# Kernel optimization log

Measured on AMD Instinct MI355X. Metric: run time of the kernel, lower is better.

## Reference

```python
import jax, jax.numpy as jnp
import numpy as np

N_HEADS = 16


def setup_inputs() -> dict:
    key = jax.random.key(0)
    ks = jax.random.split(key, 8)
    ts, td, b, hc = 64, 4096, 8, 1024
    scale = 1.0 / np.sqrt(hc)
    return {
        "s": jax.random.normal(ks[0], (ts, b, hc), dtype=jnp.float32),
        "d": jax.random.normal(ks[1], (td, b, hc), dtype=jnp.float32),
        "Wq": jax.random.normal(ks[2], (hc, hc), dtype=jnp.float32) * scale,
        "bq": jax.random.normal(ks[3], (hc,), dtype=jnp.float32) * 0.01,
        "Wk": jax.random.normal(ks[4], (hc, hc), dtype=jnp.float32) * scale,
        "bk": jax.random.normal(ks[5], (hc,), dtype=jnp.float32) * 0.01,
        "Wv": jax.random.normal(ks[6], (hc, hc), dtype=jnp.float32) * scale,
        "bv": jax.random.normal(ks[7], (hc,), dtype=jnp.float32) * 0.01,
    }


def reference(s, d, Wq, bq, Wk, bk, Wv, bv):
    ts, b, hc = s.shape
    td = d.shape[0]
    h = N_HEADS
    c = hc // h
    # linear projections (torch Linear: x @ W.T + b)
    q = (s @ Wq.T + bq).reshape(ts, b, h, c)
    k = (d @ Wk.T + bk).reshape(td, b, h, c)
    v = (d @ Wv.T + bv).reshape(td, b, h, c)
    # scores over (slot, token) pairs, scaled
    a = jnp.einsum('sbhc,dbhc->sdbh', q, k) / jnp.sqrt(jnp.asarray(c, s.dtype))
    # competitive softmax across the SLOT axis (dim 0), not the key axis
    a = jax.nn.softmax(a, axis=0)          # (ts, td, b, h)
    n = jnp.sum(a, axis=1) + 0.001         # (ts, b, h)
    num = jnp.einsum('sdbh,dbhc->sbhc', a, v)
    out = num / n[..., None]               # normalized weighted average
    return out.reshape(ts, b, hc)
```

## Files before the change

kernel.cpp:

```cpp
#include <hip/hip_runtime.h>


#define TS 64
#define TD 4096
#define BATCH 8
#define HC 1024
#define NHEAD 16
#define MD (TD*BATCH)
#define MS (TS*BATCH)
#define NCHUNK 8
#define CHTOK (TD/NCHUNK)

typedef __attribute__((ext_vector_type(8))) __bf16 bf16x8;
typedef __attribute__((ext_vector_type(4))) float f32x4;
typedef __attribute__((ext_vector_type(4))) unsigned short u16x4;
typedef __attribute__((ext_vector_type(8))) unsigned short u16x8;

__device__ __forceinline__ unsigned short f2bf(float x){
  union { float f; unsigned u; } v; v.f = x;
  unsigned r = v.u + 0x7FFFu + ((v.u >> 16) & 1u);
  return (unsigned short)(r >> 16);
}

__device__ __forceinline__ void gll16(const void* g, void* l){
  __builtin_amdgcn_global_load_lds((__attribute__((address_space(1))) void*)g,
                                   (__attribute__((address_space(3))) void*)l, 16, 0, 0);
}

__global__ void cvt_all(const float* __restrict__ d, const float* __restrict__ s,
                        const float* __restrict__ wq, const float* __restrict__ wk,
                        const float* __restrict__ wv,
                        unsigned short* __restrict__ dbf, unsigned short* __restrict__ sbf,
                        unsigned short* __restrict__ wqb, unsigned short* __restrict__ wkb,
                        unsigned short* __restrict__ wvb){
  long i = (long)blockIdx.x * 256 + threadIdx.x;
  const float* src; unsigned short* dst; long off;
  if (i < 8388608L)      { src = d;  dst = dbf; off = i; }
  else if (i < 8519680L) { src = s;  dst = sbf; off = i - 8388608L; }
  else if (i < 8781824L) { src = wq; dst = wqb; off = i - 8519680L; }
  else if (i < 9043968L) { src = wk; dst = wkb; off = i - 8781824L; }
  else                   { src = wv; dst = wvb; off = i - 9043968L; }
  f32x4 f = ((const f32x4*)src)[off];
  u16x4 o;
  o[0] = f2bf(f[0]); o[1] = f2bf(f[1]); o[2] = f2bf(f[2]); o[3] = f2bf(f[3]);
  ((u16x4*)dst)[off] = o;
}

__global__ __launch_bounds__(256, 2) void gemm_kv(
    const unsigned short* __restrict__ A,
    const unsigned short* __restrict__ W,
    const float* __restrict__ bk,
    const float* __restrict__ bv,
    unsigned short* __restrict__ Kout,
    unsigned short* __restrict__ Vout)
{
  __shared__ unsigned short As[2][256*32];
  __shared__ unsigned short Bs[2][128*32];

  const int nwg = gridDim.x;
  const int cpx = nwg >> 3;
  const int orig = blockIdx.x;
  const int wg = (orig & 7) * cpx + (orig >> 3);
  const int mt = wg >> 4, nt = wg & 15;
  const int tid = threadIdx.x;
  const int lane = tid & 63, w = tid >> 6;
  const int l15 = lane & 15, lg = lane >> 4;
  const int wm = w >> 1, wn = w & 1;

  const int srow = lane >> 2;
  const unsigned schunk = (unsigned)(((lane & 3) ^ ((lane >> 3) & 3)) << 4);
  const char* aS = (const char*)A + (size_t)(mt*256) * 2048 + schunk;
  const char* bS = (const char*)W + (size_t)(nt*128) * 2048 + schunk;
  const unsigned ar0 = (unsigned)((  0 + w*16 + srow) * 2048);
  const unsigned ar1 = (unsigned)(( 64 + w*16 + srow) * 2048);
  const unsigned ar2 = (unsigned)((128 + w*16 + srow) * 2048);
  const unsigned ar3 = (unsigned)((192 + w*16 + srow) * 2048);
  const unsigned br0 = ar0, br1 = ar1;
  const unsigned da0 = (unsigned)((  0 + w*16) * 64);
  const unsigned da1 = (unsigned)(( 64 + w*16) * 64);
  const unsigned da2 = (unsigned)((128 + w*16) * 64);
  const unsigned da3 = (unsigned)((192 + w*16) * 64);

  #define STAGE(t_, buf_) { \
    const size_t ko = (size_t)(t_) * 64; \
    char* dA = (char*)&As[buf_][0]; char* dB = (char*)&Bs[buf_][0]; \
    gll16(aS + ar0 + ko, dA + da0); \
    gll16(aS + ar1 + ko, dA + da1); \
    gll16(aS + ar2 + ko, dA + da2); \
    gll16(aS + ar3 + ko, dA + da3); \
    gll16(bS + br0 + ko, dB + da0); \
    gll16(bS + br1 + ko, dB + da1); \
    __builtin_amdgcn_sched_barrier(0); }

  const unsigned ksel = (unsigned)((lg ^ ((l15 >> 1) & 3)) << 4);
  const unsigned aoff = (unsigned)(wm*128 + l15) * 64 + ksel;
  const unsigned boff = (unsigned)(wn*64  + l15) * 64 + ksel;

  const f32x4 fz = {0.f, 0.f, 0.f, 0.f};
  f32x4 acc[8][4];
  #pragma unroll
  for (int m = 0; m < 8; ++m)
    #pragma unroll
    for (int n = 0; n < 4; ++n) acc[m][n] = fz;

  #define TILE(buf_) { \
    const char* as_ = (const char*)&As[buf_][0]; \
    const char* bs_ = (const char*)&Bs[buf_][0]; \
    bf16x8 af[8], bf[4]; \
    _Pragma("unroll") \
    for (int m = 0; m < 8; ++m) af[m] = *(const bf16x8*)(as_ + aoff + m*1024u); \
    _Pragma("unroll") \
    for (int n = 0; n < 4; ++n) bf[n] = *(const bf16x8*)(bs_ + boff + n*1024u); \
    __builtin_amdgcn_s_setprio(1); \
    _Pragma("unroll") \
    for (int m = 0; m < 8; ++m) \
      _Pragma("unroll") \
      for (int n = 0; n < 4; ++n) \
        acc[m][n] = __builtin_amdgcn_mfma_f32_16x16x32_bf16(af[m], bf[n], acc[m][n], 0, 0, 0); \
    __builtin_amdgcn_s_setprio(0); }

  STAGE(0, 0)
  __syncthreads();

  #pragma unroll 1
  for (int tp = 0; tp < 16; ++tp){
    STAGE(2*tp + 1, 1)
    TILE(0)
    __syncthreads();
    if (tp < 15) STAGE(2*tp + 2, 0)
    TILE(1)
    __syncthreads();
  }

  const int ccol = (nt & 7)*128 + wn*64;
  unsigned short* Cb = (nt < 8) ? Kout : Vout;
  const float* bias = (nt < 8) ? bk : bv;
  float bvv[4];
  #pragma unroll
  for (int nf = 0; nf < 4; ++nf) bvv[nf] = bias[ccol + nf*16 + l15];
  #pragma unroll
  for (int mf = 0; mf < 8; ++mf){
    #pragma unroll
    for (int r = 0; r < 4; ++r){
      size_t row = (size_t)(mt*256 + wm*128 + mf*16 + lg*4 + r);
      unsigned short* cp = Cb + row*1024 + ccol;
      #pragma unroll
      for (int nf = 0; nf < 4; ++nf)
        cp[nf*16 + l15] = f2bf(acc[mf][nf][r] + bvv[nf]);
    }
  }
  #undef STAGE
  #undef TILE
}

__global__ __launch_bounds__(256) void gemm128(
    const unsigned short* __restrict__ A,
    const unsigned short* __restrict__ W,
    const float* __restrict__ bias,
    unsigned short* __restrict__ C)
{
  __shared__ unsigned short As[128*64];
  __shared__ unsigned short Bs[128*64];
  const int nwg = gridDim.x;
  const int cpx = nwg >> 3;
  const int orig = blockIdx.x;
  const int wg = (orig & 7) * cpx + (orig >> 3);
  const int mt = wg >> 3, nt = wg & 7;
  const int tid = threadIdx.x;
  const int lane = tid & 63, w = tid >> 6;
  const int l15 = lane & 15, lg = lane >> 4;
  const int wr = w >> 1, wc = w & 1;

  const int lrow = lane >> 3;
  const int lch  = (lane & 7) << 4;
  const char* pA[4]; const char* pB[4]; unsigned ldsoff[4];
  #pragma unroll
  for (int j = 0; j < 4; ++j){
    int row = w*32 + j*8 + lrow;
    int sw  = lch ^ ((row & 7) << 4);
    pA[j] = (const char*)A + (size_t)(mt*128 + row) * 2048 + sw;
    pB[j] = (const char*)W + (size_t)(nt*128 + row) * 2048 + sw;
    ldsoff[j] = (unsigned)(w*32 + j*8) * 128;
  }

  const f32x4 fz = {0.f, 0.f, 0.f, 0.f};
  f32x4 acc[4][4];
  #pragma unroll
  for (int m = 0; m < 4; ++m)
    #pragma unroll
    for (int n = 0; n < 4; ++n) acc[m][n] = fz;

  for (int kt = 0; kt < 16; ++kt){
    __syncthreads();
    #pragma unroll
    for (int j = 0; j < 4; ++j){
      gll16(pA[j] + (size_t)kt*128, (char*)As + ldsoff[j]);
      gll16(pB[j] + (size_t)kt*128, (char*)Bs + ldsoff[j]);
    }
    __syncthreads();
    #pragma unroll
    for (int kk = 0; kk < 2; ++kk){
      bf16x8 af[4], bfr[4];
      #pragma unroll
      for (int m = 0; m < 4; ++m){
        int row = wr*64 + m*16 + l15;
        af[m] = *(const bf16x8*)((const char*)As + row*128 + ((lg*16 + kk*64) ^ ((row & 7) << 4)));
      }
      #pragma unroll
      for (int n = 0; n < 4; ++n){
        int row = wc*64 + n*16 + l15;
        bfr[n] = *(const bf16x8*)((const char*)Bs + row*128 + ((lg*16 + kk*64) ^ ((row & 7) << 4)));
      }
      #pragma unroll
      for (int m = 0; m < 4; ++m)
        #pragma unroll
        for (int n = 0; n < 4; ++n)
          acc[m][n] = __builtin_amdgcn_mfma_f32_16x16x32_bf16(af[m], bfr[n], acc[m][n], 0, 0, 0);
    }
  }

  const int ccol0 = nt*128 + wc*64;
  float bv[4];
  #pragma unroll
  for (int n = 0; n < 4; ++n) bv[n] = bias[ccol0 + n*16 + l15];
  #pragma unroll
  for (int m = 0; m < 4; ++m){
    #pragma unroll
    for (int r = 0; r < 4; ++r){
      size_t row = (size_t)(mt*128 + wr*64 + m*16 + lg*4 + r);
      unsigned short* cp = C + row*1024 + ccol0;
      #pragma unroll
      for (int n = 0; n < 4; ++n)
        cp[n*16 + l15] = f2bf(acc[m][n][r] + bv[n]);
    }
  }
}

__global__ __launch_bounds__(256) void attn_kernel(
    const unsigned short* __restrict__ Q,
    const unsigned short* __restrict__ K,
    const unsigned short* __restrict__ V,
    float* __restrict__ P)
{
  __shared__ unsigned short Qs[64*64];
  __shared__ unsigned short Ks[64*64];
  __shared__ unsigned short Vt[80*64];
  __shared__ unsigned short Al[64*64];
  __shared__ float red[256];

  const int bh = blockIdx.x;
  const int chunk = blockIdx.y;
  const int bb = bh >> 4, h = bh & 15;
  const int tid = threadIdx.x;
  const int lane = tid & 63, w = tid >> 6;
  const int l15 = lane & 15, lg = lane >> 4;
  const int lrow = lane >> 3, lch = (lane & 7) << 4;

  for (int i = tid; i < 16*64; i += 256){
    int r = i >> 6;
    Vt[(64 + r)*64 + (i & 63)] = (r == 0) ? (unsigned short)0x3F80 : (unsigned short)0;
  }

  #pragma unroll
  for (int j = 0; j < 2; ++j){
    int row = w*16 + j*8 + lrow;
    int sw = lch ^ ((row & 7) << 4);
    const char* g = (const char*)Q + (size_t)(row*BATCH + bb)*2048 + h*128 + sw;
    gll16(g, (char*)Qs + (w*16 + j*8)*128);
  }

  const f32x4 fz = {0.f, 0.f, 0.f, 0.f};
  f32x4 acc[5];
  #pragma unroll
  for (int nb = 0; nb < 5; ++nb) acc[nb] = fz;

  const int vtok = tid >> 2;
  const int vcg  = tid & 3;
  const int t0 = chunk * CHTOK;

  for (int tt = 0; tt < CHTOK/64; ++tt){
    const int tb = t0 + tt*64;
    #pragma unroll
    for (int j = 0; j < 2; ++j){
      int row = w*16 + j*8 + lrow;
      int sw = lch ^ ((row & 7) << 4);
      const char* g = (const char*)K + (size_t)((size_t)(tb + row)*BATCH + bb)*2048 + h*128 + sw;
      gll16(g, (char*)Ks + (w*16 + j*8)*128);
    }
    const char* vg = (const char*)V + (size_t)((size_t)(tb + vtok)*BATCH + bb)*2048 + h*128 + vcg*32;
    u16x8 v0 = *(const u16x8*)vg;
    u16x8 v1 = *(const u16x8*)(vg + 16);
    __syncthreads();

    bf16x8 qa[2];
    #pragma unroll
    for (int kk = 0; kk < 2; ++kk){
      int row = w*16 + l15;
      qa[kk] = *(const bf16x8*)((const char*)Qs + row*128 + ((lg*16 + kk*64) ^ ((row & 7) << 4)));
    }
    float e[4][4];
    #pragma unroll
    for (int nb = 0; nb < 4; ++nb){
      f32x4 s = fz;
      #pragma unroll
      for (int kk = 0; kk < 2; ++kk){
        int row = nb*16 + l15;
        bf16x8 kb = *(const bf16x8*)((const char*)Ks + row*128 + ((lg*16 + kk*64) ^ ((row & 7) << 4)));
        s = __builtin_amdgcn_mfma_f32_16x16x32_bf16(qa[kk], kb, s, 0, 0, 0);
      }
      #pragma unroll
      for (int r = 0; r < 4; ++r) e[nb][r] = __expf(s[r] * 0.125f);
    }
    #pragma unroll
    for (int nb = 0; nb < 4; ++nb){
      float cp = e[nb][0] + e[nb][1] + e[nb][2] + e[nb][3];
      cp += __shfl_xor(cp, 16);
      cp += __shfl_xor(cp, 32);
      if (lg == 0) red[w*64 + nb*16 + l15] = cp;
    }
    __syncthreads();

    #pragma unroll
    for (int nb = 0; nb < 4; ++nb){
      int col = nb*16 + l15;
      float dn = red[col] + red[64 + col] + red[128 + col] + red[192 + col];
      float inv = 1.0f / dn;
      #pragma unroll
      for (int r = 0; r < 4; ++r){
        int row = w*16 + lg*4 + r;
        Al[row*64 + ((((2*col)) ^ ((row & 7) << 4)) >> 1)] = f2bf(e[nb][r] * inv);
      }
    }
    #pragma unroll
    for (int ee = 0; ee < 8; ++ee){
      int c0 = vcg*16 + ee;
      int sw0 = (((c0 & 7) ^ (c0 >> 3)) & 7) << 4;
      Vt[c0*64 + (((2*vtok) ^ sw0) >> 1)] = v0[ee];
    }
    #pragma unroll
    for (int ee = 0; ee < 8; ++ee){
      int c1 = vcg*16 + 8 + ee;
      int sw1 = (((c1 & 7) ^ (c1 >> 3)) & 7) << 4;
      Vt[c1*64 + (((2*vtok) ^ sw1) >> 1)] = v1[ee];
    }
    __syncthreads();

    bf16x8 aa[2];
    #pragma unroll
    for (int kk = 0; kk < 2; ++kk){
      int row = w*16 + l15;
      aa[kk] = *(const bf16x8*)((const char*)Al + row*128 + ((lg*16 + kk*64) ^ ((row & 7) << 4)));
    }
    #pragma unroll
    for (int nb = 0; nb < 5; ++nb){
      #pragma unroll
      for (int kk = 0; kk < 2; ++kk){
        int row = nb*16 + l15;
        int sw = (((row & 7) ^ (row >> 3)) & 7) << 4;
        bf16x8 vb = *(const bf16x8*)((const char*)Vt + row*128 + ((lg*16 + kk*64) ^ sw));
        acc[nb] = __builtin_amdgcn_mfma_f32_16x16x32_bf16(aa[kk], vb, acc[nb], 0, 0, 0);
      }
    }
  }

  float* Pb = P + (size_t)(bh*NCHUNK + chunk) * 64 * 80;
  #pragma unroll
  for (int nb = 0; nb < 5; ++nb){
    #pragma unroll
    for (int r = 0; r < 4; ++r){
      int s = w*16 + lg*4 + r;
      Pb[(size_t)s*80 + nb*16 + l15] = acc[nb][r];
    }
  }
}

__global__ void reduce_out(const float* __restrict__ P, float* __restrict__ out){
  int flat = blockIdx.x * 256 + threadIdx.x;
  int c = flat & 63, s = (flat >> 6) & 63, bh = flat >> 12;
  int bb = bh >> 4, h = bh & 15;
  float sc = 0.f, sn = 0.f;
  #pragma unroll
  for (int ch = 0; ch < NCHUNK; ++ch){
    const float* base = P + ((size_t)(bh*NCHUNK + ch)*64 + s)*80;
    sc += base[c];
    sn += base[64];
  }
  out[((size_t)s*BATCH + bb)*1024 + h*64 + c] = sc / (sn + 0.001f);
}

extern "C" void kernel_launch(void* const* d_in, const int* in_sizes, int n_in,
                              void* d_out, int out_size, void* d_ws, size_t ws_size,
                              hipStream_t stream)
{
  const float* s  = (const float*)d_in[0];
  const float* d  = (const float*)d_in[1];
  const float* Wq = (const float*)d_in[2];
  const float* bq = (const float*)d_in[3];
  const float* Wk = (const float*)d_in[4];
  const float* bk = (const float*)d_in[5];
  const float* Wv = (const float*)d_in[6];
  const float* bv = (const float*)d_in[7];
  float* out = (float*)d_out;

  char* ws = (char*)d_ws;
  unsigned short* dbf = (unsigned short*)(ws);
  unsigned short* sbf = (unsigned short*)(ws + 67108864);
  unsigned short* wqb = (unsigned short*)(ws + 68157440);
  unsigned short* wkb = (unsigned short*)(ws + 70254592);
  unsigned short* wvb = (unsigned short*)(ws + 72351744);
  unsigned short* Qw  = (unsigned short*)(ws + 74448896);
  unsigned short* Kw  = (unsigned short*)(ws + 75497472);
  unsigned short* Vw  = (unsigned short*)(ws + 142606336);
  float*          Pw  = (float*)(ws + 209715200);

  (void)in_sizes; (void)n_in; (void)out_size; (void)ws_size;

  cvt_all<<<36352, 256, 0, stream>>>(d, s, Wq, Wk, Wv, dbf, sbf, wqb, wkb, wvb);

  gemm128<<<(MS/128)*8, 256, 0, stream>>>(sbf, wqb, bq, Qw);
  gemm_kv<<<(MD/256)*16, 256, 0, stream>>>(dbf, wkb, bk, bv, Kw, Vw);

  attn_kernel<<<dim3(128, NCHUNK), 256, 0, stream>>>(Qw, Kw, Vw, Pw);

  reduce_out<<<(TS*BATCH*HC)/256, 256, 0, stream>>>(Pw, out);
}
```

Before: 254.4 us.

## Widen KV GEMM tile to 256x256 with 512 threads computing K and V together

```diff
diff --git a/kernel.cpp b/kernel.cpp
--- a/kernel.cpp
+++ b/kernel.cpp
@@ -46,50 +46,48 @@
   ((u16x4*)dst)[off] = o;
 }
 
-__global__ __launch_bounds__(256, 2) void gemm_kv(
+__global__ __launch_bounds__(512, 2) void gemm_kv(
     const unsigned short* __restrict__ A,
-    const unsigned short* __restrict__ W,
+    const unsigned short* __restrict__ Wkv,
     const float* __restrict__ bk,
     const float* __restrict__ bv,
     unsigned short* __restrict__ Kout,
     unsigned short* __restrict__ Vout)
 {
   __shared__ unsigned short As[2][256*32];
-  __shared__ unsigned short Bs[2][128*32];
+  __shared__ unsigned short Bs[2][256*32];
 
   const int nwg = gridDim.x;
   const int cpx = nwg >> 3;
   const int orig = blockIdx.x;
   const int wg = (orig & 7) * cpx + (orig >> 3);
-  const int mt = wg >> 4, nt = wg & 15;
+  const int mt = wg >> 3, nt = wg & 7;
   const int tid = threadIdx.x;
   const int lane = tid & 63, w = tid >> 6;
   const int l15 = lane & 15, lg = lane >> 4;
-  const int wm = w >> 1, wn = w & 1;
-
-  const int srow = lane >> 2;
-  const unsigned schunk = (unsigned)(((lane & 3) ^ ((lane >> 3) & 3)) << 4);
-  const char* aS = (const char*)A + (size_t)(mt*256) * 2048 + schunk;
-  const char* bS = (const char*)W + (size_t)(nt*128) * 2048 + schunk;
-  const unsigned ar0 = (unsigned)((  0 + w*16 + srow) * 2048);
-  const unsigned ar1 = (unsigned)(( 64 + w*16 + srow) * 2048);
-  const unsigned ar2 = (unsigned)((128 + w*16 + srow) * 2048);
-  const unsigned ar3 = (unsigned)((192 + w*16 + srow) * 2048);
-  const unsigned br0 = ar0, br1 = ar1;
-  const unsigned da0 = (unsigned)((  0 + w*16) * 64);
-  const unsigned da1 = (unsigned)(( 64 + w*16) * 64);
-  const unsigned da2 = (unsigned)((128 + w*16) * 64);
-  const unsigned da3 = (unsigned)((192 + w*16) * 64);
+  const int wm = w >> 2, wn = w & 3;
+
+  const int r4 = lane >> 2;
+  const unsigned sw4 = (unsigned)(((lane & 3) ^ ((lane >> 3) & 3)) << 4);
+  size_t a_src[2]; size_t b_src[2]; unsigned s_dst[2];
+  #pragma unroll
+  for (int j = 0; j < 2; ++j){
+    int la = w*32 + j*16 + r4;
+    a_src[j] = (size_t)(mt*256 + la) * 2048 + sw4;
+    int gb = (la < 128) ? (nt*128 + la) : (1024 + nt*128 + (la - 128));
+    b_src[j] = (size_t)gb * 2048 + sw4;
+    s_dst[j] = (unsigned)((w*32 + j*16) * 64);
+  }
+  const char* aP = (const char*)A;
+  const char* bP = (const char*)Wkv;
 
   #define STAGE(t_, buf_) { \
     const size_t ko = (size_t)(t_) * 64; \
-    char* dA = (char*)&As[buf_][0]; char* dB = (char*)&Bs[buf_][0]; \
-    gll16(aS + ar0 + ko, dA + da0); \
-    gll16(aS + ar1 + ko, dA + da1); \
-    gll16(aS + ar2 + ko, dA + da2); \
-    gll16(aS + ar3 + ko, dA + da3); \
-    gll16(bS + br0 + ko, dB + da0); \
-    gll16(bS + br1 + ko, dB + da1); \
+    char* dA_ = (char*)&As[buf_][0]; char* dB_ = (char*)&Bs[buf_][0]; \
+    gll16(aP + a_src[0] + ko, dA_ + s_dst[0]); \
+    gll16(aP + a_src[1] + ko, dA_ + s_dst[1]); \
+    gll16(bP + b_src[0] + ko, dB_ + s_dst[0]); \
+    gll16(bP + b_src[1] + ko, dB_ + s_dst[1]); \
     __builtin_amdgcn_sched_barrier(0); }
 
   const unsigned ksel = (unsigned)((lg ^ ((l15 >> 1) & 3)) << 4);
@@ -106,17 +104,17 @@
   #define TILE(buf_) { \
     const char* as_ = (const char*)&As[buf_][0]; \
     const char* bs_ = (const char*)&Bs[buf_][0]; \
-    bf16x8 af[8], bf[4]; \
+    bf16x8 af[8], bfr[4]; \
     _Pragma("unroll") \
     for (int m = 0; m < 8; ++m) af[m] = *(const bf16x8*)(as_ + aoff + m*1024u); \
     _Pragma("unroll") \
-    for (int n = 0; n < 4; ++n) bf[n] = *(const bf16x8*)(bs_ + boff + n*1024u); \
+    for (int n = 0; n < 4; ++n) bfr[n] = *(const bf16x8*)(bs_ + boff + n*1024u); \
     __builtin_amdgcn_s_setprio(1); \
     _Pragma("unroll") \
     for (int m = 0; m < 8; ++m) \
       _Pragma("unroll") \
       for (int n = 0; n < 4; ++n) \
-        acc[m][n] = __builtin_amdgcn_mfma_f32_16x16x32_bf16(af[m], bf[n], acc[m][n], 0, 0, 0); \
+        acc[m][n] = __builtin_amdgcn_mfma_f32_16x16x32_bf16(af[m], bfr[n], acc[m][n], 0, 0, 0); \
     __builtin_amdgcn_s_setprio(0); }
 
   STAGE(0, 0)
@@ -132,9 +130,9 @@
     __syncthreads();
   }
 
-  const int ccol = (nt & 7)*128 + wn*64;
-  unsigned short* Cb = (nt < 8) ? Kout : Vout;
-  const float* bias = (nt < 8) ? bk : bv;
+  const int ccol = nt*128 + (wn & 1)*64;
+  unsigned short* Cb = (wn < 2) ? Kout : Vout;
+  const float* bias = (wn < 2) ? bk : bv;
   float bvv[4];
   #pragma unroll
   for (int nf = 0; nf < 4; ++nf) bvv[nf] = bias[ccol + nf*16 + l15];
@@ -418,7 +416,7 @@
   cvt_all<<<36352, 256, 0, stream>>>(d, s, Wq, Wk, Wv, dbf, sbf, wqb, wkb, wvb);
 
   gemm128<<<(MS/128)*8, 256, 0, stream>>>(sbf, wqb, bq, Qw);
-  gemm_kv<<<(MD/256)*16, 256, 0, stream>>>(dbf, wkb, bk, bv, Kw, Vw);
+  gemm_kv<<<(MD/256)*8, 512, 0, stream>>>(dbf, wkb, bk, bv, Kw, Vw);
 
   attn_kernel<<<dim3(128, NCHUNK), 256, 0, stream>>>(Qw, Kw, Vw, Pw);
 
```

Result: slower. 264.7 us (+4.0%).
